# Performance work log

Measured on AMD Instinct MI355X. Metric: run time of the kernel, lower is better.

The kernel has to match this reference:

```python
import jax, jax.numpy as jnp
import numpy as np

W, L, K, N = 32, 64, 512, 64


def setup_inputs() -> dict:
    key = jax.random.key(0)
    k0, k1, k2, k3 = jax.random.split(key, 4)
    # 0/1 spin states stored as float, matching torch.randint(0, 2, ..., dtype=float32)
    states = jax.random.randint(k0, (W, L, K, N), 0, 2).astype(jnp.float32)
    Q = jax.random.normal(k1, (W, N, N), dtype=jnp.float32)
    # inverse temperatures, ascending (standard parallel-tempering ladder)
    beta = jnp.sort(jax.random.uniform(k2, (L,), minval=0.1, maxval=2.0, dtype=jnp.float32))
    # uniform draws replacing torch.rand_like(delta) in exchange()
    u = jax.random.uniform(k3, (W, L - 1, K), dtype=jnp.float32)
    return {"states": states, "Q": Q, "beta": beta, "u": u}


def reference(states, Q, beta, u):
    """Temperer.exchange(): energies then masked replica swap.

    Returns (energies (W,L,K) before exchange, new states (W,L,K,N)).
    """
    # energy: einsum('wlki,wij,wlkj->wlk') done as one GEMM + elementwise reduce
    sQ = jnp.einsum('wlki,wij->wlkj', states, Q)          # (W,L,K,N)
    energies = jnp.einsum('wlkj,wlkj->wlk', sQ, states)   # (W,L,K)

    dbeta = (beta[1:] - beta[:-1])[None, :, None]          # (1,L-1,1)
    delta = (energies[:, 1:] - energies[:, :-1]) * dbeta   # (W,L-1,K)
    mask = (u < jnp.exp(delta)).astype(states.dtype)[..., None]  # (W,L-1,K,1)

    left = states[:, :-1]
    right = states[:, 1:]
    # replicate torch's sequential overlapping slice assignments exactly
    new = states.at[:, :-1].set(mask * right + (1.0 - mask) * left)
    new = new.at[:, 1:].set(mask * left + (1.0 - mask) * right)
    return energies, new
```

## Files before the change

### kernel.cpp

```cpp
#include <hip/hip_runtime.h>
#include <math.h>

#define PW 32
#define PL 64
#define PK 512
#define PN 64

typedef int v4i __attribute__((ext_vector_type(4)));


constexpr int TILES_PER_WAVE = 8;

__global__ __launch_bounds__(256) void energies_kernel(
    const float* __restrict__ states, const float* __restrict__ Q,
    float* __restrict__ e_out, double* __restrict__ e64)
{
    __shared__ alignas(16) signed char Afrag[20 * 64 * 16];

    const int tid  = threadIdx.x;
    const int lane = tid & 63;
    const int wv   = tid >> 6;
    const int w    = blockIdx.x >> 6;
    const int blk  = blockIdx.x & 63;

    const float* Qw = Q + w * PN * PN;
    for (int e = tid; e < PN * PN; e += 256) {
        const int i = e >> 6, j = e & 63;
        long long R = llrint((double)Qw[e] * 8589934592.0);
        const int frag_lane = ((i >> 4) << 4) | (j & 15);
        const int jt = j >> 4;
        const int b  = i & 15;
#pragma unroll
        for (int k = 0; k < 5; ++k) {
            const signed char d = (signed char)(R & 0xFF);
            R = (R - d) >> 8;
            Afrag[((k * 4 + jt) * 64 + frag_lane) * 16 + b] = d;
        }
    }
    __syncthreads();

    const v4i* Af = (const v4i*)Afrag;

    const long vw_base = (long)w * (PL * PK)
                       + (long)(blk * 4 + wv) * (16 * TILES_PER_WAVE);

    for (int t = 0; t < TILES_PER_WAVE; ++t) {
        const long vbase = vw_base + (long)t * 16;
        const float* sp = states + vbase * PN + lane;

        unsigned long long mk = 0;
#pragma unroll
        for (int v = 0; v < 16; ++v) {
            const float s = sp[v * PN];
            const unsigned long long m = __ballot(s != 0.0f);
            mk = ((lane & 15) == v) ? m : mk;
        }

        const unsigned int bits16 =
            (unsigned int)(mk >> ((lane >> 4) * 16)) & 0xFFFFu;
        v4i B;
#pragma unroll
        for (int q = 0; q < 4; ++q)
            B[q] = (int)((((bits16 >> (4 * q)) & 0xFu) * 0x00204081u) & 0x01010101u);

        int selb[4];
#pragma unroll
        for (int jt = 0; jt < 4; ++jt)
            selb[jt] = (int)((mk >> (jt * 16 + ((lane >> 4) * 4))) & 0xF);

        long long acc = 0;
#pragma unroll
        for (int k = 0; k < 5; ++k) {
            v4i A0 = Af[(k * 4 + 0) * 64 + lane];
            v4i A1 = Af[(k * 4 + 1) * 64 + lane];
            v4i A2 = Af[(k * 4 + 2) * 64 + lane];
            v4i A3 = Af[(k * 4 + 3) * 64 + lane];
            v4i C0 = {0, 0, 0, 0}, C1 = {0, 0, 0, 0};
            v4i C2 = {0, 0, 0, 0}, C3 = {0, 0, 0, 0};
            asm("s_nop 1\n\t"
                "v_mfma_i32_16x16x64_i8 %0, %4, %8, %0\n\t"
                "v_mfma_i32_16x16x64_i8 %1, %5, %8, %1\n\t"
                "v_mfma_i32_16x16x64_i8 %2, %6, %8, %2\n\t"
                "v_mfma_i32_16x16x64_i8 %3, %7, %8, %3\n\t"
                "s_nop 7\n\t"
                "s_nop 7"
                : "+v"(C0), "+v"(C1), "+v"(C2), "+v"(C3)
                : "v"(A0), "v"(A1), "v"(A2), "v"(A3), "v"(B));
            int ak = 0;
#pragma unroll
            for (int r = 0; r < 4; ++r) {
                ak += ((selb[0] >> r) & 1) * C0[r];
                ak += ((selb[1] >> r) & 1) * C1[r];
                ak += ((selb[2] >> r) & 1) * C2[r];
                ak += ((selb[3] >> r) & 1) * C3[r];
            }
            acc += (long long)ak << (8 * k);
        }

        acc += __shfl_xor(acc, 16, 64);
        acc += __shfl_xor(acc, 32, 64);

        if (lane < 16) {
            const double e = (double)acc * 0x1p-33;
            e64[vbase + lane]   = e;
            e_out[vbase + lane] = (float)e;
        }
    }
}

__global__ __launch_bounds__(256) void mask_kernel(
    const double* __restrict__ e64, const float* __restrict__ beta,
    const float* __restrict__ u, unsigned char* __restrict__ mask)
{
    const int idx = blockIdx.x * blockDim.x + threadIdx.x;
    if (idx >= PW * (PL - 1) * PK) return;
    const int k = idx % PK;
    const int m = (idx / PK) % (PL - 1);
    const int w = idx / (PK * (PL - 1));
    const long e1 = ((long)w * PL + m) * PK + k;
    const double db = (double)beta[m + 1] - (double)beta[m];
    const double delta = (e64[e1 + PK] - e64[e1]) * db;
    mask[idx] = ((double)u[idx] < exp(delta)) ? 1 : 0;
}

__global__ __launch_bounds__(256) void swap_kernel(
    const float* __restrict__ states, const unsigned char* __restrict__ mask,
    float* __restrict__ out)
{
    const long rowBase = (long)blockIdx.x * 32;
    const int w  = (int)(rowBase >> 15);
    const int l  = (int)((rowBase >> 9) & 63);
    const int k0 = (int)(rowBase & 511);

    const int tid = threadIdx.x;
    const int r  = tid >> 3;
    const int j4 = tid & 7;
    const int k  = k0 + r;

    const int ml = (l == 0) ? 0 : (l - 1);
    const unsigned char mk = mask[((long)w * (PL - 1) + ml) * PK + k];
    int sl;
    if (l == 0) sl = mk ? 1 : 0;
    else        sl = mk ? (l - 1) : l;

    const float4* srcp = (const float4*)(states + (((long)w * PL + sl) * PK + k) * PN);
    float4*       dstp = (float4*)(out + (rowBase + r) * PN);
    dstp[j4]     = srcp[j4];
    dstp[j4 + 8] = srcp[j4 + 8];
}

extern "C" void kernel_launch(void* const* d_in, const int* in_sizes, int n_in,
                              void* d_out, int out_size, void* d_ws, size_t ws_size,
                              hipStream_t stream) {
    const float* states = (const float*)d_in[0];
    const float* Q      = (const float*)d_in[1];
    const float* beta   = (const float*)d_in[2];
    const float* u      = (const float*)d_in[3];

    float* e_out      = (float*)d_out;
    float* new_states = (float*)d_out + (long)PW * PL * PK;

    double* e64 = (double*)d_ws;
    unsigned char* mask = (unsigned char*)d_ws + sizeof(double) * (long)PW * PL * PK;

    energies_kernel<<<2048, 256, 0, stream>>>(states, Q, e_out, e64);

    const int nmask = PW * (PL - 1) * PK;
    mask_kernel<<<(nmask + 255) / 256, 256, 0, stream>>>(e64, beta, u, mask);

    swap_kernel<<<32768, 256, 0, stream>>>(states, mask, new_states);
}
```

Before: 504.2 us.

## Cut Q fixed-point to 4 int8 limbs, pair tiles per MFMA pass, nontemporal swap stores

Lowers the fixed-point scale for Q from 2^33 to 2^28 so it splits into four int8 limbs instead of five, removing one limb's worth of MFMA work and LDS fragments. Each wave now handles two 16-replica tiles per iteration, so every A fragment loaded from LDS feeds two MFMAs and the per-block s_nop padding is shared across twice the work. The swap kernel writes its output with nontemporal stores to avoid polluting the cache. The lower scale reduces the precision of the energies, which could flip swap decisions near the acceptance threshold, and the paired tiles raise register pressure.

```diff
diff --git a/kernel.cpp b/kernel.cpp
--- a/kernel.cpp
+++ b/kernel.cpp
@@ -6,16 +6,17 @@
 #define PK 512
 #define PN 64
 
-typedef int v4i __attribute__((ext_vector_type(4)));
+typedef int   v4i __attribute__((ext_vector_type(4)));
+typedef float v4f __attribute__((ext_vector_type(4)));
 
 
-constexpr int TILES_PER_WAVE = 8;
+constexpr int ITERS_PER_WAVE = 4;
 
 __global__ __launch_bounds__(256) void energies_kernel(
     const float* __restrict__ states, const float* __restrict__ Q,
     float* __restrict__ e_out, double* __restrict__ e64)
 {
-    __shared__ alignas(16) signed char Afrag[20 * 64 * 16];
+    __shared__ alignas(16) signed char Afrag[16 * 64 * 16];
 
     const int tid  = threadIdx.x;
     const int lane = tid & 63;
@@ -26,12 +27,12 @@
     const float* Qw = Q + w * PN * PN;
     for (int e = tid; e < PN * PN; e += 256) {
         const int i = e >> 6, j = e & 63;
-        long long R = llrint((double)Qw[e] * 8589934592.0);
+        long long R = llrint((double)Qw[e] * 268435456.0);
         const int frag_lane = ((i >> 4) << 4) | (j & 15);
         const int jt = j >> 4;
         const int b  = i & 15;
 #pragma unroll
-        for (int k = 0; k < 5; ++k) {
+        for (int k = 0; k < 4; ++k) {
             const signed char d = (signed char)(R & 0xFF);
             R = (R - d) >> 8;
             Afrag[((k * 4 + jt) * 64 + frag_lane) * 16 + b] = d;
@@ -42,68 +43,92 @@
     const v4i* Af = (const v4i*)Afrag;
 
     const long vw_base = (long)w * (PL * PK)
-                       + (long)(blk * 4 + wv) * (16 * TILES_PER_WAVE);
+                       + (long)(blk * 4 + wv) * (32 * ITERS_PER_WAVE);
 
-    for (int t = 0; t < TILES_PER_WAVE; ++t) {
-        const long vbase = vw_base + (long)t * 16;
+    for (int t = 0; t < ITERS_PER_WAVE; ++t) {
+        const long vbase = vw_base + (long)t * 32;
         const float* sp = states + vbase * PN + lane;
 
-        unsigned long long mk = 0;
+        unsigned long long mkA = 0, mkB = 0;
 #pragma unroll
         for (int v = 0; v < 16; ++v) {
-            const float s = sp[v * PN];
-            const unsigned long long m = __ballot(s != 0.0f);
-            mk = ((lane & 15) == v) ? m : mk;
+            const float sA = sp[v * PN];
+            const float sB = sp[(v + 16) * PN];
+            const unsigned long long mA = __ballot(sA != 0.0f);
+            const unsigned long long mB = __ballot(sB != 0.0f);
+            const bool sel = (lane & 15) == v;
+            mkA = sel ? mA : mkA;
+            mkB = sel ? mB : mkB;
         }
 
-        const unsigned int bits16 =
-            (unsigned int)(mk >> ((lane >> 4) * 16)) & 0xFFFFu;
-        v4i B;
+        const int sh = (lane >> 4) * 16;
+        const unsigned int bA = (unsigned int)(mkA >> sh) & 0xFFFFu;
+        const unsigned int bB = (unsigned int)(mkB >> sh) & 0xFFFFu;
+        v4i BA, BB;
 #pragma unroll
-        for (int q = 0; q < 4; ++q)
-            B[q] = (int)((((bits16 >> (4 * q)) & 0xFu) * 0x00204081u) & 0x01010101u);
+        for (int q = 0; q < 4; ++q) {
+            BA[q] = (int)((((bA >> (4 * q)) & 0xFu) * 0x00204081u) & 0x01010101u);
+            BB[q] = (int)((((bB >> (4 * q)) & 0xFu) * 0x00204081u) & 0x01010101u);
+        }
 
-        int selb[4];
+        int selA[4], selB[4];
 #pragma unroll
-        for (int jt = 0; jt < 4; ++jt)
-            selb[jt] = (int)((mk >> (jt * 16 + ((lane >> 4) * 4))) & 0xF);
+        for (int jt = 0; jt < 4; ++jt) {
+            selA[jt] = (int)((mkA >> (jt * 16 + ((lane >> 4) * 4))) & 0xF);
+            selB[jt] = (int)((mkB >> (jt * 16 + ((lane >> 4) * 4))) & 0xF);
+        }
 
-        long long acc = 0;
+        long long accA = 0, accB = 0;
 #pragma unroll
-        for (int k = 0; k < 5; ++k) {
+        for (int k = 0; k < 4; ++k) {
             v4i A0 = Af[(k * 4 + 0) * 64 + lane];
             v4i A1 = Af[(k * 4 + 1) * 64 + lane];
             v4i A2 = Af[(k * 4 + 2) * 64 + lane];
             v4i A3 = Af[(k * 4 + 3) * 64 + lane];
-            v4i C0 = {0, 0, 0, 0}, C1 = {0, 0, 0, 0};
-            v4i C2 = {0, 0, 0, 0}, C3 = {0, 0, 0, 0};
+            v4i CA0 = {0,0,0,0}, CA1 = {0,0,0,0}, CA2 = {0,0,0,0}, CA3 = {0,0,0,0};
+            v4i CB0 = {0,0,0,0}, CB1 = {0,0,0,0}, CB2 = {0,0,0,0}, CB3 = {0,0,0,0};
             asm("s_nop 1\n\t"
-                "v_mfma_i32_16x16x64_i8 %0, %4, %8, %0\n\t"
-                "v_mfma_i32_16x16x64_i8 %1, %5, %8, %1\n\t"
-                "v_mfma_i32_16x16x64_i8 %2, %6, %8, %2\n\t"
-                "v_mfma_i32_16x16x64_i8 %3, %7, %8, %3\n\t"
+                "v_mfma_i32_16x16x64_i8 %0, %8, %12, %0\n\t"
+                "v_mfma_i32_16x16x64_i8 %4, %8, %13, %4\n\t"
+                "v_mfma_i32_16x16x64_i8 %1, %9, %12, %1\n\t"
+                "v_mfma_i32_16x16x64_i8 %5, %9, %13, %5\n\t"
+                "v_mfma_i32_16x16x64_i8 %2, %10, %12, %2\n\t"
+                "v_mfma_i32_16x16x64_i8 %6, %10, %13, %6\n\t"
+                "v_mfma_i32_16x16x64_i8 %3, %11, %12, %3\n\t"
+                "v_mfma_i32_16x16x64_i8 %7, %11, %13, %7\n\t"
                 "s_nop 7\n\t"
                 "s_nop 7"
-                : "+v"(C0), "+v"(C1), "+v"(C2), "+v"(C3)
-                : "v"(A0), "v"(A1), "v"(A2), "v"(A3), "v"(B));
-            int ak = 0;
+                : "+v"(CA0), "+v"(CA1), "+v"(CA2), "+v"(CA3),
+                  "+v"(CB0), "+v"(CB1), "+v"(CB2), "+v"(CB3)
+                : "v"(A0), "v"(A1), "v"(A2), "v"(A3), "v"(BA), "v"(BB));
+            int akA = 0, akB = 0;
 #pragma unroll
             for (int r = 0; r < 4; ++r) {
-                ak += ((selb[0] >> r) & 1) * C0[r];
-                ak += ((selb[1] >> r) & 1) * C1[r];
-                ak += ((selb[2] >> r) & 1) * C2[r];
-                ak += ((selb[3] >> r) & 1) * C3[r];
+                akA += ((selA[0] >> r) & 1) * CA0[r];
+                akA += ((selA[1] >> r) & 1) * CA1[r];
+                akA += ((selA[2] >> r) & 1) * CA2[r];
+                akA += ((selA[3] >> r) & 1) * CA3[r];
+                akB += ((selB[0] >> r) & 1) * CB0[r];
+                akB += ((selB[1] >> r) & 1) * CB1[r];
+                akB += ((selB[2] >> r) & 1) * CB2[r];
+                akB += ((selB[3] >> r) & 1) * CB3[r];
             }
-            acc += (long long)ak << (8 * k);
+            accA += (long long)akA << (8 * k);
+            accB += (long long)akB << (8 * k);
         }
 
-        acc += __shfl_xor(acc, 16, 64);
-        acc += __shfl_xor(acc, 32, 64);
+        accA += __shfl_xor(accA, 16, 64);
+        accA += __shfl_xor(accA, 32, 64);
+        accB += __shfl_xor(accB, 16, 64);
+        accB += __shfl_xor(accB, 32, 64);
 
         if (lane < 16) {
-            const double e = (double)acc * 0x1p-33;
-            e64[vbase + lane]   = e;
-            e_out[vbase + lane] = (float)e;
+            const double eA = (double)accA * 0x1p-28;
+            const double eB = (double)accB * 0x1p-28;
+            e64[vbase + lane]        = eA;
+            e_out[vbase + lane]      = (float)eA;
+            e64[vbase + 16 + lane]   = eB;
+            e_out[vbase + 16 + lane] = (float)eB;
         }
     }
 }
@@ -143,10 +168,10 @@
     if (l == 0) sl = mk ? 1 : 0;
     else        sl = mk ? (l - 1) : l;
 
-    const float4* srcp = (const float4*)(states + (((long)w * PL + sl) * PK + k) * PN);
-    float4*       dstp = (float4*)(out + (rowBase + r) * PN);
-    dstp[j4]     = srcp[j4];
-    dstp[j4 + 8] = srcp[j4 + 8];
+    const v4f* srcp = (const v4f*)(states + (((long)w * PL + sl) * PK + k) * PN);
+    v4f*       dstp = (v4f*)(out + (rowBase + r) * PN);
+    __builtin_nontemporal_store(srcp[j4],     &dstp[j4]);
+    __builtin_nontemporal_store(srcp[j4 + 8], &dstp[j4 + 8]);
 }
 
 extern "C" void kernel_launch(void* const* d_in, const int* in_sizes, int n_in,
```

Result: slower. 523.8 us (+3.9%).
